# Kernel tuning notes

Measured on AMD Instinct MI355X. Metric: run time of the kernel, lower is better.

## Reference

```python
import jax, jax.numpy as jnp
import numpy as np

# Complete 32-ary tree of depth 3: vocab = 32**3 = 32768 leaves.
B = 4096       # batch
NHID = 512     # hidden size
BR = 32        # branching factor (num_children at every internal node)
DEPTH = 3      # number of internal-node decisions from root to leaf
V = BR ** DEPTH
NUM_NODES = sum(BR ** k for k in range(DEPTH))  # 1 + 32 + 1024 = 1057

# Static tree-indexing tables (level-order node numbering).
_LEVEL_OFFSET = np.array([sum(BR ** j for j in range(k)) for k in range(DEPTH)], dtype=np.int64)   # [0, 1, 33]
_NODE_DIV = np.array([BR ** (DEPTH - k) for k in range(DEPTH)], dtype=np.int64)                    # node-within-level divisor
_STEP_DIV = np.array([BR ** (DEPTH - 1 - k) for k in range(DEPTH)], dtype=np.int64)                # child-step divisor


def setup_inputs() -> dict:
    key = jax.random.key(0)
    k1, k2, k3 = jax.random.split(key, 3)
    inputs = jax.random.normal(k1, (B, NHID), dtype=jnp.float32)
    labels = jax.random.randint(k2, (B,), 0, V)                     # leaf index per sample
    W = jax.random.normal(k3, (NUM_NODES, NHID, BR), dtype=jnp.float32)  # all node params, stacked
    return {"inputs": inputs, "labels": labels, "W": W}


def reference(inputs, labels, W):
    lab = labels[:, None]                                            # [B, 1]
    node_idx = jnp.asarray(_LEVEL_OFFSET)[None, :] + lab // jnp.asarray(_NODE_DIV)[None, :]  # [B, D] node on path
    steps = (lab // jnp.asarray(_STEP_DIV)[None, :]) % BR            # [B, D] child taken at each node
    Wg = W[node_idx]                                                 # [B, D, NHID, BR] gathered path params
    logits = jnp.einsum('bh,bdhc->bdc', inputs, Wg)                  # [B, D, BR]
    p = jax.nn.softmax(logits, axis=-1)
    step_p = jnp.take_along_axis(p, steps[:, :, None], axis=-1)[..., 0]  # [B, D]
    return jnp.prod(step_p, axis=-1)                                 # [B] path probability
```

## Files before the change

kernel.cpp:

```cpp
#include <hip/hip_runtime.h>


#define NHID  512
#define BR    32
#define BATCH 4096
#define NBUCK 1024
#define SMAX  8
#define SCAP  64

__device__ __forceinline__ float dpp_xadd1(float v) {
    int m = __builtin_amdgcn_update_dpp(0, __float_as_int(v), 0xB1, 0xF, 0xF, true);
    return v + __int_as_float(m);
}
__device__ __forceinline__ float dpp_xadd2(float v) {
    int m = __builtin_amdgcn_update_dpp(0, __float_as_int(v), 0x4E, 0xF, 0xF, true);
    return v + __int_as_float(m);
}

#define FMA4(A, xv, wv_) do { \
    (A).x = fmaf((xv), (wv_).x, (A).x); \
    (A).y = fmaf((xv), (wv_).y, (A).y); \
    (A).z = fmaf((xv), (wv_).z, (A).z); \
    (A).w = fmaf((xv), (wv_).w, (A).w); } while (0)

__global__ __launch_bounds__(256, 4) void hsm_fused(
    const float* __restrict__ inputs,
    const int* __restrict__ labels,
    const float* __restrict__ W,
    float* __restrict__ out)
{
    __shared__ float xsT[NHID * SMAX];
    __shared__ float partial[8 * SMAX * 8 * 4];
    __shared__ float pk[3][SMAX];
    __shared__ int   slist[SCAP];
    __shared__ int   scount;

    const int g   = blockIdx.x;
    const int tid = threadIdx.x;

    if (tid == 0) scount = 0;
    __syncthreads();

    #pragma unroll
    for (int r = 0; r < BATCH / 256; ++r) {
        int j = tid + 256 * r;
        int lab = labels[j];
        if ((lab >> 5) == g) {
            int p = atomicAdd(&scount, 1);
            if (p < SCAP) slist[p] = (j << 5) | (lab & 31);
        }
    }
    __syncthreads();
    const int n = min(scount, SCAP);
    if (n == 0) return;

    const int wv   = tid >> 6;
    const int lane = tid & 63;
    const int hsel = lane & 7;
    const int colg = lane >> 3;

    const int node1 = 1 + (g >> 5);
    const int node2 = 33 + g;

    for (int c0 = 0; c0 < n; c0 += SMAX) {
        const int m = min(SMAX, n - c0);

        __syncthreads();
        #pragma unroll
        for (int r = 0; r < 2; ++r) {
            int h = tid + 256 * r;
            float vals[SMAX];
            #pragma unroll
            for (int s = 0; s < SMAX; ++s) {
                float v = 0.0f;
                if (s < m) {
                    int sid = slist[c0 + s] >> 5;
                    v = inputs[(size_t)sid * NHID + h];
                }
                vals[s] = v;
            }
            float4* dst = (float4*)&xsT[h * SMAX];
            dst[0] = make_float4(vals[0], vals[1], vals[2], vals[3]);
            dst[1] = make_float4(vals[4], vals[5], vals[6], vals[7]);
        }
        __syncthreads();

        #pragma unroll
        for (int k = 0; k < 3; ++k) {
            const int node = (k == 0) ? 0 : (k == 1) ? node1 : node2;

            const float4* wp = (const float4*)(W + (size_t)node * (NHID * BR))
                               + wv * 1024 + hsel * 8 + colg;
            const float4* xp = (const float4*)xsT + (128 * wv + hsel) * 2;

            float4 acc[SMAX];
            #pragma unroll
            for (int s = 0; s < SMAX; ++s) acc[s] = make_float4(0, 0, 0, 0);

            #pragma unroll 4
            for (int i = 0; i < 16; ++i) {
                float4 w4 = wp[i * 64];
                float4 xa = xp[i * 16];
                float4 xb = xp[i * 16 + 1];
                FMA4(acc[0], xa.x, w4); FMA4(acc[1], xa.y, w4);
                FMA4(acc[2], xa.z, w4); FMA4(acc[3], xa.w, w4);
                FMA4(acc[4], xb.x, w4); FMA4(acc[5], xb.y, w4);
                FMA4(acc[6], xb.z, w4); FMA4(acc[7], xb.w, w4);
            }

            #pragma unroll
            for (int s = 0; s < SMAX; ++s) {
                acc[s].x = dpp_xadd2(dpp_xadd1(acc[s].x));
                acc[s].y = dpp_xadd2(dpp_xadd1(acc[s].y));
                acc[s].z = dpp_xadd2(dpp_xadd1(acc[s].z));
                acc[s].w = dpp_xadd2(dpp_xadd1(acc[s].w));
            }
            if ((lane & 3) == 0) {
                int wq = wv * 2 + ((lane >> 2) & 1);
                #pragma unroll
                for (int s = 0; s < SMAX; ++s)
                    *(float4*)&partial[((wq * SMAX + s) * 8 + colg) * 4] = acc[s];
            }
            __syncthreads();

            {
                int s   = tid >> 5;
                int col = tid & 31;
                int cg  = col >> 2, cc = col & 3;
                float l = 0.0f;
                #pragma unroll
                for (int wq = 0; wq < 8; ++wq)
                    l += partial[((wq * SMAX + s) * 8 + cg) * 4 + cc];
                float mx = l;
                #pragma unroll
                for (int mm = 1; mm <= 16; mm <<= 1)
                    mx = fmaxf(mx, __shfl_xor(mx, mm));
                float e = expf(l - mx);
                float es = e;
                #pragma unroll
                for (int mm = 1; mm <= 16; mm <<= 1)
                    es += __shfl_xor(es, mm);
                int step = (k == 0) ? (g >> 5)
                         : (k == 1) ? (g & 31)
                                    : (slist[c0 + s] & 31);
                if (col == step) pk[k][s] = e / es;
            }
            __syncthreads();
        }

        if (tid < m) {
            int sid = slist[c0 + tid] >> 5;
            out[sid] = pk[0][tid] * pk[1][tid] * pk[2][tid];
        }
    }
}

extern "C" void kernel_launch(void* const* d_in, const int* in_sizes, int n_in,
                              void* d_out, int out_size, void* d_ws, size_t ws_size,
                              hipStream_t stream)
{
    const float* inputs = (const float*)d_in[0];
    const int*   labels = (const int*)d_in[1];
    const float* W      = (const float*)d_in[2];
    float* out = (float*)d_out;

    hsm_fused<<<dim3(NBUCK), dim3(256), 0, stream>>>(inputs, labels, W, out);
}
```

Baseline: 126.8 us.

## Fuse three tree-level matvecs into one pass with smaller sample tile

Sample tile size per chunk drops from 8 to 4. All three node weight matrices (root, level-1, level-2) are now accumulated in a single loop that shares one x load per iteration. The per-level barriers and partial-sum round trips collapse into one reduction stage and one softmax stage covering all three levels. The aim is to cut synchronisation and to overlap the three weight streams. In exchange, buckets with more than 4 samples need more chunks, so weights are re-read more often, and register pressure rises with 48 accumulators.

```diff
diff --git a/kernel.cpp b/kernel.cpp
--- a/kernel.cpp
+++ b/kernel.cpp
@@ -5,7 +5,7 @@
 #define BR    32
 #define BATCH 4096
 #define NBUCK 1024
-#define SMAX  8
+#define SMAX  4
 #define SCAP  64
 
 __device__ __forceinline__ float dpp_xadd1(float v) {
@@ -30,7 +30,7 @@
     float* __restrict__ out)
 {
     __shared__ float xsT[NHID * SMAX];
-    __shared__ float partial[8 * SMAX * 8 * 4];
+    __shared__ float partial[8 * 3 * SMAX * BR];
     __shared__ float pk[3][SMAX];
     __shared__ int   slist[SCAP];
     __shared__ int   scount;
@@ -62,6 +62,12 @@
     const int node1 = 1 + (g >> 5);
     const int node2 = 33 + g;
 
+    const size_t laneoff = (size_t)wv * 1024 + hsel * 8 + colg;
+    const float4* wp0 = (const float4*)W + laneoff;
+    const float4* wp1 = (const float4*)(W + (size_t)node1 * (NHID * BR)) + laneoff;
+    const float4* wp2 = (const float4*)(W + (size_t)node2 * (NHID * BR)) + laneoff;
+    const float4* xs4 = (const float4*)xsT;
+
     for (int c0 = 0; c0 < n; c0 += SMAX) {
         const int m = min(SMAX, n - c0);
 
@@ -69,68 +75,70 @@
         #pragma unroll
         for (int r = 0; r < 2; ++r) {
             int h = tid + 256 * r;
-            float vals[SMAX];
+            float v[SMAX];
             #pragma unroll
             for (int s = 0; s < SMAX; ++s) {
-                float v = 0.0f;
+                float x = 0.0f;
                 if (s < m) {
                     int sid = slist[c0 + s] >> 5;
-                    v = inputs[(size_t)sid * NHID + h];
+                    x = inputs[(size_t)sid * NHID + h];
                 }
-                vals[s] = v;
+                v[s] = x;
             }
-            float4* dst = (float4*)&xsT[h * SMAX];
-            dst[0] = make_float4(vals[0], vals[1], vals[2], vals[3]);
-            dst[1] = make_float4(vals[4], vals[5], vals[6], vals[7]);
+            ((float4*)xsT)[h] = make_float4(v[0], v[1], v[2], v[3]);
         }
         __syncthreads();
 
+        float4 acc[3][SMAX];
+        #pragma unroll
+        for (int k = 0; k < 3; ++k)
+            #pragma unroll
+            for (int s = 0; s < SMAX; ++s) acc[k][s] = make_float4(0, 0, 0, 0);
+
+        #pragma unroll 4
+        for (int i = 0; i < 16; ++i) {
+            float4 w0 = wp0[i * 64];
+            float4 w1 = wp1[i * 64];
+            float4 w2 = wp2[i * 64];
+            float4 x4 = xs4[wv * 128 + i * 8 + hsel];
+            FMA4(acc[0][0], x4.x, w0); FMA4(acc[0][1], x4.y, w0);
+            FMA4(acc[0][2], x4.z, w0); FMA4(acc[0][3], x4.w, w0);
+            FMA4(acc[1][0], x4.x, w1); FMA4(acc[1][1], x4.y, w1);
+            FMA4(acc[1][2], x4.z, w1); FMA4(acc[1][3], x4.w, w1);
+            FMA4(acc[2][0], x4.x, w2); FMA4(acc[2][1], x4.y, w2);
+            FMA4(acc[2][2], x4.z, w2); FMA4(acc[2][3], x4.w, w2);
+        }
+
         #pragma unroll
         for (int k = 0; k < 3; ++k) {
-            const int node = (k == 0) ? 0 : (k == 1) ? node1 : node2;
-
-            const float4* wp = (const float4*)(W + (size_t)node * (NHID * BR))
-                               + wv * 1024 + hsel * 8 + colg;
-            const float4* xp = (const float4*)xsT + (128 * wv + hsel) * 2;
-
-            float4 acc[SMAX];
-            #pragma unroll
-            for (int s = 0; s < SMAX; ++s) acc[s] = make_float4(0, 0, 0, 0);
-
-            #pragma unroll 4
-            for (int i = 0; i < 16; ++i) {
-                float4 w4 = wp[i * 64];
-                float4 xa = xp[i * 16];
-                float4 xb = xp[i * 16 + 1];
-                FMA4(acc[0], xa.x, w4); FMA4(acc[1], xa.y, w4);
-                FMA4(acc[2], xa.z, w4); FMA4(acc[3], xa.w, w4);
-                FMA4(acc[4], xb.x, w4); FMA4(acc[5], xb.y, w4);
-                FMA4(acc[6], xb.z, w4); FMA4(acc[7], xb.w, w4);
-            }
-
             #pragma unroll
             for (int s = 0; s < SMAX; ++s) {
-                acc[s].x = dpp_xadd2(dpp_xadd1(acc[s].x));
-                acc[s].y = dpp_xadd2(dpp_xadd1(acc[s].y));
-                acc[s].z = dpp_xadd2(dpp_xadd1(acc[s].z));
-                acc[s].w = dpp_xadd2(dpp_xadd1(acc[s].w));
+                acc[k][s].x = dpp_xadd2(dpp_xadd1(acc[k][s].x));
+                acc[k][s].y = dpp_xadd2(dpp_xadd1(acc[k][s].y));
+                acc[k][s].z = dpp_xadd2(dpp_xadd1(acc[k][s].z));
+                acc[k][s].w = dpp_xadd2(dpp_xadd1(acc[k][s].w));
             }
-            if ((lane & 3) == 0) {
-                int wq = wv * 2 + ((lane >> 2) & 1);
+        }
+        if ((lane & 3) == 0) {
+            int wq = wv * 2 + ((lane >> 2) & 1);
+            #pragma unroll
+            for (int k = 0; k < 3; ++k)
                 #pragma unroll
                 for (int s = 0; s < SMAX; ++s)
-                    *(float4*)&partial[((wq * SMAX + s) * 8 + colg) * 4] = acc[s];
-            }
-            __syncthreads();
+                    *(float4*)&partial[((wq * 3 + k) * SMAX + s) * BR + colg * 4]
+                        = acc[k][s];
+        }
+        __syncthreads();
 
-            {
-                int s   = tid >> 5;
-                int col = tid & 31;
-                int cg  = col >> 2, cc = col & 3;
+        if (tid < 32 * SMAX) {
+            int s   = tid >> 5;
+            int col = tid & 31;
+            #pragma unroll
+            for (int k = 0; k < 3; ++k) {
                 float l = 0.0f;
                 #pragma unroll
                 for (int wq = 0; wq < 8; ++wq)
-                    l += partial[((wq * SMAX + s) * 8 + cg) * 4 + cc];
+                    l += partial[((wq * 3 + k) * SMAX + s) * BR + col];
                 float mx = l;
                 #pragma unroll
                 for (int mm = 1; mm <= 16; mm <<= 1)
@@ -145,8 +153,8 @@
                                     : (slist[c0 + s] & 31);
                 if (col == step) pk[k][s] = e / es;
             }
-            __syncthreads();
         }
+        __syncthreads();
 
         if (tid < m) {
             int sid = slist[c0 + tid] >> 5;
```

Result: slower. 150.5 us (+18.7%).
